# Kernel tuning notes

Measured on AMD Instinct MI355X. Metric: run time of the kernel, lower is better.

## Reference

```python
import jax, jax.numpy as jnp
import numpy as np

# Circuit structure constants (must match input_specs)
V, K, C = 128, 32, 256   # vars, input nodes per var, categories (V*K == N)
L, N, F = 4, 4096, 16    # layer pairs, sum nodes per layer, sum fan-in
E, B = 8192, 512         # product elements per layer, batch size
EPS = 1e-6


def setup_inputs() -> dict:
    key = jax.random.key(0)
    ks = jax.random.split(key, 6)
    return {
        "inputs": jax.random.randint(ks[0], (B, V), 0, C),
        "prod_child_ids": jax.random.randint(ks[1], (L, E, 2), 0, N),
        "sum_child_ids": jax.random.randint(ks[2], (L, N, F), 0, E),
        "input_params": jax.random.uniform(ks[3], (V, K, C), dtype=jnp.float32),
        "sum_params": jax.random.uniform(ks[4], (L, N, F), dtype=jnp.float32),
        "root_params": jax.random.uniform(ks[5], (N,), dtype=jnp.float32),
    }


def _forward(inputs, prod_child_ids, sum_child_ids, input_params, sum_params, root_params):
    # --- input layer: categorical leaves -> node_mars [V*K, B] (log space) ---
    lw_in = jnp.log(input_params + EPS)
    lw_in = lw_in - jax.nn.logsumexp(lw_in, axis=-1, keepdims=True)  # normalized log-params
    x = inputs.T  # [V, B]
    nm = lw_in[jnp.arange(V)[:, None, None], jnp.arange(K)[None, :, None], x[:, None, :]]  # [V, K, B]
    nm = nm.reshape(V * K, B)  # node_mars for leaves, V*K == N

    # --- normalized sum-layer log-weights ---
    lw_sum = jnp.log(sum_params + EPS)
    lw_sum = lw_sum - jax.nn.logsumexp(lw_sum, axis=-1, keepdims=True)  # [L, N, F]

    # --- alternating prod / sum layer groups (fixed small L) ---
    for l in range(L):
        # product layer: element_mars[e] = sum of child node_mars (log space add)
        em = nm[prod_child_ids[l, :, 0]] + nm[prod_child_ids[l, :, 1]]  # [E, B]
        # sum layer: node_mars[n] = logsumexp_j(element_mars[child j] + log w[n, j])
        ch = em[sum_child_ids[l]]  # [N, F, B] irregular gather
        nm = jax.nn.logsumexp(ch + lw_sum[l][:, :, None], axis=1)  # [N, B]

    # --- root sum node -> log-likelihoods [B] ---
    lr = jnp.log(root_params + EPS)
    lr = lr - jax.nn.logsumexp(lr)
    return jax.nn.logsumexp(nm + lr[:, None], axis=0)  # [B]


def reference(inputs, prod_child_ids, sum_child_ids, input_params, sum_params, root_params):
    return _forward(inputs, prod_child_ids, sum_child_ids, input_params, sum_params, root_params)
```

## Files before the change

### kernel.cpp

```cpp
#include <hip/hip_runtime.h>
#include <hip/hip_fp16.h>
#include <math.h>

#define V_ 128
#define K_ 32
#define C_ 256
#define L_ 4
#define N_ 4096
#define F_ 16
#define E_ 8192
#define B_ 512
#define EPS_ 1e-6f

__device__ __forceinline__ __half2 u2h(unsigned u) {
    __half2 h; *reinterpret_cast<unsigned*>(&h) = u; return h;
}
__device__ __forceinline__ unsigned h2u(__half2 h) {
    return *reinterpret_cast<unsigned*>(&h);
}
__device__ __forceinline__ __half2 hmax2(__half2 a, __half2 b) {
    float2 fa = __half22float2(a), fb = __half22float2(b);
    return __floats2half2_rn(fmaxf(fa.x, fb.x), fmaxf(fa.y, fb.y));
}

__global__ __launch_bounds__(256) void prep_kernel(const float* __restrict__ sp,
                                                   const int* __restrict__ prod,
                                                   const int* __restrict__ sc,
                                                   const float* __restrict__ ip,
                                                   const float* __restrict__ rp,
                                                   unsigned* __restrict__ PU,
                                                   __half* __restrict__ PW,
                                                   float* __restrict__ inv_row,
                                                   float* __restrict__ lrpsum) {
    int blk = blockIdx.x;
    int tid = threadIdx.x;
    if (blk < 64) {
        int idx = blk * 256 + tid;
        int l   = idx >> 12;
        int n   = idx & (N_ - 1);
        const float4* row4 = (const float4*)(sp + (size_t)idx * F_);
        float v[F_];
        float s = 0.f;
#pragma unroll
        for (int q = 0; q < 4; q++) {
            float4 r = row4[q];
            v[4*q+0] = r.x + EPS_; v[4*q+1] = r.y + EPS_;
            v[4*q+2] = r.z + EPS_; v[4*q+3] = r.w + EPS_;
            s += v[4*q+0] + v[4*q+1] + v[4*q+2] + v[4*q+3];
        }
        float inv = 1.f / s;
        const int* scr = sc + (size_t)idx * F_;
#pragma unroll
        for (int f = 0; f < F_; f++) {
            int  e = scr[f];
            int2 c = ((const int2*)prod)[(size_t)l * E_ + e];
            PU[((size_t)l * F_ + f) * N_ + n] = (unsigned)c.x | ((unsigned)c.y << 16);
            PW[((size_t)l * F_ + f) * N_ + n] = __float2half(v[f] * inv);
        }
    } else if (blk < 64 + 1024) {
        int rblk = blk - 64;
        int n    = rblk * 4 + (tid >> 6);
        int lane = tid & 63;
        const float* row = ip + (size_t)n * C_;
        float t = 0.f;
#pragma unroll
        for (int i = 0; i < 4; i++) t += row[lane + 64 * i] + EPS_;
#pragma unroll
        for (int off = 32; off; off >>= 1) t += __shfl_down(t, off, 64);
        if (lane == 0) inv_row[n] = 1.f / t;
    } else {
        __shared__ float smem[4];
        float acc = 0.f;
        for (int i = tid; i < N_; i += 256) acc += rp[i] + EPS_;
#pragma unroll
        for (int off = 32; off; off >>= 1) acc += __shfl_down(acc, off, 64);
        if ((tid & 63) == 0) smem[tid >> 6] = acc;
        __syncthreads();
        if (tid == 0) lrpsum[0] = __logf(smem[0] + smem[1] + smem[2] + smem[3]);
    }
}

__global__ __launch_bounds__(1024) void mega_kernel(const float* __restrict__ ip,
                                                    const int* __restrict__ inputs,
                                                    const float* __restrict__ inv_row,
                                                    const float* __restrict__ rp,
                                                    const unsigned* __restrict__ PU,
                                                    const __half* __restrict__ PW,
                                                    const float* __restrict__ lrpsum,
                                                    float* __restrict__ out) {
    __shared__ unsigned nm[N_];
    __shared__ unsigned redm[16];
    __shared__ float    redf[32];
    int tid  = threadIdx.x;
    int lane = tid & 63;
    int w    = tid >> 6;
    int b0   = blockIdx.x * 2, b1 = b0 + 1;

    float2 u[4];
    float mx0 = 0.f, mx1 = 0.f;
#pragma unroll
    for (int p = 0; p < 4; p++) {
        int n  = p * 1024 + tid;
        int v  = n >> 5;
        int x0 = inputs[b0 * V_ + v];
        int x1 = inputs[b1 * V_ + v];
        float invr = inv_row[n];
        u[p].x = (ip[(size_t)n * C_ + x0] + EPS_) * invr;
        u[p].y = (ip[(size_t)n * C_ + x1] + EPS_) * invr;
        mx0 = fmaxf(mx0, u[p].x);
        mx1 = fmaxf(mx1, u[p].y);
    }
#pragma unroll
    for (int off = 32; off; off >>= 1) {
        mx0 = fmaxf(mx0, __shfl_down(mx0, off, 64));
        mx1 = fmaxf(mx1, __shfl_down(mx1, off, 64));
    }
    if (lane == 0) { redf[w] = mx0; redf[16 + w] = mx1; }
    __syncthreads();
    float m0 = redf[0], m1 = redf[16];
#pragma unroll
    for (int i = 1; i < 16; i++) { m0 = fmaxf(m0, redf[i]); m1 = fmaxf(m1, redf[16 + i]); }
    float inv0 = 1.f / m0, inv1 = 1.f / m1;
    float sg0 = -__logf(inv0), sg1 = -__logf(inv1);
#pragma unroll
    for (int p = 0; p < 4; p++)
        nm[p * 1024 + tid] = h2u(__floats2half2_rn(u[p].x * inv0, u[p].y * inv1));
    __syncthreads();

    for (int l = 0; l < L_ - 1; l++) {
        const unsigned* pu = PU + (size_t)l * F_ * N_;
        const __half*   pw = PW + (size_t)l * F_ * N_;
        unsigned o[4];
        __half2  hm = u2h(0u);
#pragma unroll
        for (int p = 0; p < 4; p++) {
            int n = p * 1024 + tid;
            unsigned pk[F_];
            __half   wv[F_];
#pragma unroll
            for (int f = 0; f < F_; f++) { pk[f] = pu[f * N_ + n]; wv[f] = pw[f * N_ + n]; }
            __half2 acc = u2h(0u);
#pragma unroll
            for (int f = 0; f < F_; f++) {
                __half2 a = u2h(nm[pk[f] & 0xffff]);
                __half2 b = u2h(nm[pk[f] >> 16]);
                acc = __hfma2(__hmul2(a, b), __half2half2(wv[f]), acc);
            }
            o[p] = h2u(acc);
            hm   = hmax2(hm, acc);
        }
#pragma unroll
        for (int off = 32; off; off >>= 1)
            hm = hmax2(hm, u2h(__shfl_down(h2u(hm), off, 64)));
        if (lane == 0) redm[w] = h2u(hm);
        __syncthreads();
        __half2 M = u2h(redm[0]);
#pragma unroll
        for (int i = 1; i < 16; i++) M = hmax2(M, u2h(redm[i]));
        float M0 = __half2float(__low2half(M)), M1 = __half2float(__high2half(M));
        __half2 hi = __floats2half2_rn(1.f / M0, 1.f / M1);
        float ai0 = __half2float(__low2half(hi)), ai1 = __half2float(__high2half(hi));
        sg0 = 2.f * sg0 - __logf(ai0);
        sg1 = 2.f * sg1 - __logf(ai1);
#pragma unroll
        for (int p = 0; p < 4; p++)
            nm[p * 1024 + tid] = h2u(__hmul2(u2h(o[p]), hi));
        __syncthreads();
    }

    {
        const unsigned* pu = PU + (size_t)(L_ - 1) * F_ * N_;
        const __half*   pw = PW + (size_t)(L_ - 1) * F_ * N_;
        float S0 = 0.f, S1 = 0.f;
#pragma unroll
        for (int p = 0; p < 4; p++) {
            int n = p * 1024 + tid;
            unsigned pk[F_];
            __half   wv[F_];
#pragma unroll
            for (int f = 0; f < F_; f++) { pk[f] = pu[f * N_ + n]; wv[f] = pw[f * N_ + n]; }
            __half2 acc = u2h(0u);
#pragma unroll
            for (int f = 0; f < F_; f++) {
                __half2 a = u2h(nm[pk[f] & 0xffff]);
                __half2 b = u2h(nm[pk[f] >> 16]);
                acc = __hfma2(__hmul2(a, b), __half2half2(wv[f]), acc);
            }
            float2 vv = __half22float2(acc);
            float  r  = rp[n] + EPS_;
            S0 += r * vv.x;
            S1 += r * vv.y;
        }
        float sgf0 = 2.f * sg0, sgf1 = 2.f * sg1;
#pragma unroll
        for (int off = 32; off; off >>= 1) {
            S0 += __shfl_down(S0, off, 64);
            S1 += __shfl_down(S1, off, 64);
        }
        if (lane == 0) { redf[w] = S0; redf[16 + w] = S1; }
        __syncthreads();
        if (tid == 0) {
            float s0 = 0.f, s1 = 0.f;
#pragma unroll
            for (int i = 0; i < 16; i++) { s0 += redf[i]; s1 += redf[16 + i]; }
            float lr = lrpsum[0];
            out[b0] = __logf(s0) + sgf0 - lr;
            out[b1] = __logf(s1) + sgf1 - lr;
        }
    }
}

extern "C" void kernel_launch(void* const* d_in, const int* in_sizes, int n_in,
                              void* d_out, int out_size, void* d_ws, size_t ws_size,
                              hipStream_t stream) {
    const int*   inputs = (const int*)d_in[0];
    const int*   prod   = (const int*)d_in[1];
    const int*   sc     = (const int*)d_in[2];
    const float* ip     = (const float*)d_in[3];
    const float* sp     = (const float*)d_in[4];
    const float* rp     = (const float*)d_in[5];
    float* out = (float*)d_out;

    unsigned* PU      = (unsigned*)d_ws;
    __half*   PW      = (__half*)(PU + (size_t)L_ * F_ * N_);
    float*    inv_row = (float*)(PW + (size_t)L_ * F_ * N_);
    float*    lrpsum  = inv_row + N_;

    prep_kernel<<<64 + 1024 + 1, 256, 0, stream>>>(sp, prod, sc, ip, rp,
                                                   PU, PW, inv_row, lrpsum);
    mega_kernel<<<B_ / 2, 1024, 0, stream>>>(ip, inputs, inv_row, rp,
                                             PU, PW, lrpsum, out);
}
```

Measured before the change: 114.6 us.

## Materialize product layer in shared memory and pack sum child index with weight

Instead of recomputing each product element for every sum-node edge, each layer first computes all product elements into a shared-memory array, and the sum layer then gathers from it. The sum-layer metadata packs the element index and fp16 weight into one 32-bit word, replacing two global loads per edge with one. This cuts the shared-memory gathers per edge from two to one and removes a multiply. In exchange it adds a product pass with its own barrier, 32 KB of extra shared memory per block, and a second prep section that packs the product child ids.

```diff
diff --git a/kernel.cpp b/kernel.cpp
--- a/kernel.cpp
+++ b/kernel.cpp
@@ -18,6 +18,12 @@
 __device__ __forceinline__ unsigned h2u(__half2 h) {
     return *reinterpret_cast<unsigned*>(&h);
 }
+__device__ __forceinline__ __half b2h(unsigned short u) {
+    __half h; *reinterpret_cast<unsigned short*>(&h) = u; return h;
+}
+__device__ __forceinline__ unsigned short h2b(__half h) {
+    return *reinterpret_cast<unsigned short*>(&h);
+}
 __device__ __forceinline__ __half2 hmax2(__half2 a, __half2 b) {
     float2 fa = __half22float2(a), fb = __half22float2(b);
     return __floats2half2_rn(fmaxf(fa.x, fb.x), fmaxf(fa.y, fb.y));
@@ -28,8 +34,8 @@
                                                    const int* __restrict__ sc,
                                                    const float* __restrict__ ip,
                                                    const float* __restrict__ rp,
-                                                   unsigned* __restrict__ PU,
-                                                   __half* __restrict__ PW,
+                                                   unsigned* __restrict__ PIW,
+                                                   unsigned* __restrict__ PP,
                                                    float* __restrict__ inv_row,
                                                    float* __restrict__ lrpsum) {
     int blk = blockIdx.x;
@@ -52,13 +58,16 @@
         const int* scr = sc + (size_t)idx * F_;
 #pragma unroll
         for (int f = 0; f < F_; f++) {
-            int  e = scr[f];
-            int2 c = ((const int2*)prod)[(size_t)l * E_ + e];
-            PU[((size_t)l * F_ + f) * N_ + n] = (unsigned)c.x | ((unsigned)c.y << 16);
-            PW[((size_t)l * F_ + f) * N_ + n] = __float2half(v[f] * inv);
-        }
-    } else if (blk < 64 + 1024) {
-        int rblk = blk - 64;
+            unsigned wbits = h2b(__float2half(v[f] * inv));
+            PIW[((size_t)l * F_ + f) * N_ + n] =
+                (unsigned)(unsigned short)scr[f] | (wbits << 16);
+        }
+    } else if (blk < 192) {
+        int idx = (blk - 64) * 256 + tid;
+        int2 c  = ((const int2*)prod)[idx];
+        PP[idx] = (unsigned)c.x | ((unsigned)c.y << 16);
+    } else if (blk < 192 + 1024) {
+        int rblk = blk - 192;
         int n    = rblk * 4 + (tid >> 6);
         int lane = tid & 63;
         const float* row = ip + (size_t)n * C_;
@@ -84,11 +93,12 @@
                                                     const int* __restrict__ inputs,
                                                     const float* __restrict__ inv_row,
                                                     const float* __restrict__ rp,
-                                                    const unsigned* __restrict__ PU,
-                                                    const __half* __restrict__ PW,
+                                                    const unsigned* __restrict__ PIW,
+                                                    const unsigned* __restrict__ PP,
                                                     const float* __restrict__ lrpsum,
                                                     float* __restrict__ out) {
     __shared__ unsigned nm[N_];
+    __shared__ unsigned em[E_];
     __shared__ unsigned redm[16];
     __shared__ float    redf[32];
     int tid  = threadIdx.x;
@@ -128,24 +138,29 @@
     __syncthreads();
 
     for (int l = 0; l < L_ - 1; l++) {
-        const unsigned* pu = PU + (size_t)l * F_ * N_;
-        const __half*   pw = PW + (size_t)l * F_ * N_;
+        const unsigned* pp = PP + (size_t)l * E_;
+#pragma unroll
+        for (int p = 0; p < 8; p++) {
+            int e = p * 1024 + tid;
+            unsigned c = pp[e];
+            em[e] = h2u(__hmul2(u2h(nm[c & 0xffff]), u2h(nm[c >> 16])));
+        }
+        __syncthreads();
+
+        const unsigned* piw = PIW + (size_t)l * F_ * N_;
         unsigned o[4];
         __half2  hm = u2h(0u);
 #pragma unroll
         for (int p = 0; p < 4; p++) {
             int n = p * 1024 + tid;
-            unsigned pk[F_];
-            __half   wv[F_];
-#pragma unroll
-            for (int f = 0; f < F_; f++) { pk[f] = pu[f * N_ + n]; wv[f] = pw[f * N_ + n]; }
+            unsigned q[F_];
+#pragma unroll
+            for (int f = 0; f < F_; f++) q[f] = piw[f * N_ + n];
             __half2 acc = u2h(0u);
 #pragma unroll
-            for (int f = 0; f < F_; f++) {
-                __half2 a = u2h(nm[pk[f] & 0xffff]);
-                __half2 b = u2h(nm[pk[f] >> 16]);
-                acc = __hfma2(__hmul2(a, b), __half2half2(wv[f]), acc);
-            }
+            for (int f = 0; f < F_; f++)
+                acc = __hfma2(u2h(em[q[f] & 0xffff]),
+                              __half2half2(b2h((unsigned short)(q[f] >> 16))), acc);
             o[p] = h2u(acc);
             hm   = hmax2(hm, acc);
         }
@@ -169,23 +184,28 @@
     }
 
     {
-        const unsigned* pu = PU + (size_t)(L_ - 1) * F_ * N_;
-        const __half*   pw = PW + (size_t)(L_ - 1) * F_ * N_;
+        const unsigned* pp = PP + (size_t)(L_ - 1) * E_;
+#pragma unroll
+        for (int p = 0; p < 8; p++) {
+            int e = p * 1024 + tid;
+            unsigned c = pp[e];
+            em[e] = h2u(__hmul2(u2h(nm[c & 0xffff]), u2h(nm[c >> 16])));
+        }
+        __syncthreads();
+
+        const unsigned* piw = PIW + (size_t)(L_ - 1) * F_ * N_;
         float S0 = 0.f, S1 = 0.f;
 #pragma unroll
         for (int p = 0; p < 4; p++) {
             int n = p * 1024 + tid;
-            unsigned pk[F_];
-            __half   wv[F_];
-#pragma unroll
-            for (int f = 0; f < F_; f++) { pk[f] = pu[f * N_ + n]; wv[f] = pw[f * N_ + n]; }
+            unsigned q[F_];
+#pragma unroll
+            for (int f = 0; f < F_; f++) q[f] = piw[f * N_ + n];
             __half2 acc = u2h(0u);
 #pragma unroll
-            for (int f = 0; f < F_; f++) {
-                __half2 a = u2h(nm[pk[f] & 0xffff]);
-                __half2 b = u2h(nm[pk[f] >> 16]);
-                acc = __hfma2(__hmul2(a, b), __half2half2(wv[f]), acc);
-            }
+            for (int f = 0; f < F_; f++)
+                acc = __hfma2(u2h(em[q[f] & 0xffff]),
+                              __half2half2(b2h((unsigned short)(q[f] >> 16))), acc);
             float2 vv = __half22float2(acc);
             float  r  = rp[n] + EPS_;
             S0 += r * vv.x;
@@ -221,13 +241,13 @@
     const float* rp     = (const float*)d_in[5];
     float* out = (float*)d_out;
 
-    unsigned* PU      = (unsigned*)d_ws;
-    __half*   PW      = (__half*)(PU + (size_t)L_ * F_ * N_);
-    float*    inv_row = (float*)(PW + (size_t)L_ * F_ * N_);
+    unsigned* PIW     = (unsigned*)d_ws;
+    unsigned* PP      = PIW + (size_t)L_ * F_ * N_;
+    float*    inv_row = (float*)(PP + (size_t)L_ * E_);
     float*    lrpsum  = inv_row + N_;
 
-    prep_kernel<<<64 + 1024 + 1, 256, 0, stream>>>(sp, prod, sc, ip, rp,
-                                                   PU, PW, inv_row, lrpsum);
+    prep_kernel<<<64 + 128 + 1024 + 1, 256, 0, stream>>>(sp, prod, sc, ip, rp,
+                                                         PIW, PP, inv_row, lrpsum);
     mega_kernel<<<B_ / 2, 1024, 0, stream>>>(ip, inputs, inv_row, rp,
-                                             PU, PW, lrpsum, out);
-}
+                                             PIW, PP, lrpsum, out);
+}
```

After: 108.0 us. 5.7% less time.
